# Kernel tuning notes

Hardware: AMD Instinct MI355X
Metric: run time of the kernel (lower is better)

The kernel has to match this reference:

```python
import jax, jax.numpy as jnp
import numpy as np

N = 4096      # sentences in document
K = 32        # clusters (args.k)
D = 256       # input_dim
H = 128       # hidden_dim
P_SAL = 0.5   # args.percent_sal


def setup_inputs() -> dict:
    key = jax.random.key(0)
    ks = jax.random.split(key, 12)
    s = 1.0 / np.sqrt(H)
    inp = {
        "sent_gae_embeds": jax.random.normal(ks[0], (N, D), jnp.float32),
        "labels": jax.random.randint(ks[1], (N,), 0, K),
        # GRU layer 0 (torch gate order r,z,n)
        "W_ih0": jax.random.uniform(ks[2], (3 * H, D), jnp.float32, -s, s),
        "W_hh0": jax.random.uniform(ks[3], (3 * H, H), jnp.float32, -s, s),
        "b_ih0": jax.random.uniform(ks[4], (3 * H,), jnp.float32, -s, s),
        "b_hh0": jax.random.uniform(ks[5], (3 * H,), jnp.float32, -s, s),
        # GRU layer 1
        "W_ih1": jax.random.uniform(ks[6], (3 * H, H), jnp.float32, -s, s),
        "W_hh1": jax.random.uniform(ks[7], (3 * H, H), jnp.float32, -s, s),
        "b_ih1": jax.random.uniform(ks[8], (3 * H,), jnp.float32, -s, s),
        "b_hh1": jax.random.uniform(ks[9], (3 * H,), jnp.float32, -s, s),
        # weight-normed linear: W = g * v / ||v|| (norm over input dim)
        "lin_v": jax.random.normal(ks[10], (1, D + H), jnp.float32) * 0.05,
        "lin_g": jnp.ones((1, 1), jnp.float32),
        "lin_b": jnp.zeros((1,), jnp.float32),
    }
    return inp


def _gru_layer(x, W_ih, W_hh, b_ih, b_hh):
    # x: [T, B, Din] -> outputs [T, B, H]
    xw = jnp.einsum("tbd,gd->tbg", x, W_ih) + b_ih  # precompute input gates

    def step(h, xw_t):
        hw = h @ W_hh.T + b_hh
        r = jax.nn.sigmoid(xw_t[:, :H] + hw[:, :H])
        z = jax.nn.sigmoid(xw_t[:, H:2 * H] + hw[:, H:2 * H])
        n = jnp.tanh(xw_t[:, 2 * H:] + r * hw[:, 2 * H:])
        h_new = (1.0 - z) * n + z * h
        return h_new, h_new

    h0 = jnp.zeros((x.shape[1], H), x.dtype)
    _, outs = jax.lax.scan(step, h0, xw)
    return outs


def reference(sent_gae_embeds, labels, W_ih0, W_hh0, b_ih0, b_hh0,
              W_ih1, W_hh1, b_ih1, b_hh1, lin_v, lin_g, lin_b):
    # --- cluster gather: position of each sentence within its cluster ---
    onehot = jax.nn.one_hot(labels, K, dtype=jnp.int32)          # [N, K]
    pos = jnp.cumsum(onehot, axis=0)[jnp.arange(N), labels] - 1  # [N]
    lengths = onehot.sum(axis=0)                                 # [K]

    # padded per-cluster sequences: [T=N, B=K, D]
    padded = jnp.zeros((N, K, D), sent_gae_embeds.dtype).at[pos, labels].set(sent_gae_embeds)

    # --- 2-layer GRU over each cluster sequence ---
    h1 = _gru_layer(padded, W_ih0, W_hh0, b_ih0, b_hh0)
    h2 = _gru_layer(h1, W_ih1, W_hh1, b_ih1, b_hh1)
    len_c = jnp.maximum(lengths, 1)  # empty cluster -> length-1 zero sequence
    cluster_embeds = h2[len_c - 1, jnp.arange(K)]  # [K, H]

    # --- scatter cluster embeds back onto sentences (sent detached as in torch) ---
    sent_d = jax.lax.stop_gradient(sent_gae_embeds)
    final_embeds = jnp.concatenate([sent_d, cluster_embeds[labels]], axis=-1)  # [N, D+H]

    # weight-normed linear + tanh
    Wn = lin_g * lin_v / jnp.linalg.norm(lin_v, axis=1, keepdims=True)
    scores = jnp.tanh(final_embeds @ Wn.T + lin_b)[:, 0]  # [N]

    # salience: per-cluster segment-sum normalization
    clu_scores = jax.ops.segment_sum(scores, labels, num_segments=K)
    sal_scores = scores / clu_scores[labels]

    # position scores: max(0.5, exp(-(i+1)/n**(1/3)))
    inv = np.float32(1.0 / (N ** (1.0 / 3.0)))
    pos_scores = jnp.maximum(0.5, jnp.exp(-(jnp.arange(N, dtype=jnp.float32) + 1.0) * inv))

    return P_SAL * sal_scores + (1.0 - P_SAL) * pos_scores
```

## Files before the change

kernel.cpp:

```cpp
#include <hip/hip_runtime.h>
#include <cmath>

#define NN 4096
#define KK 32
#define DD 256
#define HH 128
#define G3 384
#define CH 16
#define RH 136

typedef __attribute__((ext_vector_type(8))) _Float16 h8;
typedef __attribute__((ext_vector_type(4))) float f32x4;

__device__ __forceinline__ void bar_lds() {
  asm volatile("s_waitcnt lgkmcnt(0)" ::: "memory");
  __builtin_amdgcn_s_barrier();
}

__global__ __launch_bounds__(256) void prep_k(
    const int* __restrict__ labels, const float* __restrict__ lin_v,
    const float* __restrict__ lin_g,
    const float* __restrict__ Whh0, const float* __restrict__ Wih1,
    const float* __restrict__ Whh1,
    const float* __restrict__ sent, const float* __restrict__ W_ih0,
    const float* __restrict__ b_ih0,
    int* __restrict__ order, int* __restrict__ len, float* __restrict__ scale,
    _Float16* __restrict__ P, float* __restrict__ xw,
    float* __restrict__ sdot) {
  const int blk = blockIdx.x;
  const int t = threadIdx.x;
  if (blk < 72) {
    const int gid = blk * 256 + t;
    const int lane = gid & 63;
    const int kt = (gid >> 6) & 3;
    const int nt = (gid >> 8) % 24;
    const int mat = (gid >> 8) / 24;
    const float* W = (mat == 0) ? Whh0 : (mat == 1 ? Wih1 : Whh1);
    const int n = nt * 16 + (lane & 15);
    const int kbase = kt * 32 + (lane >> 4) * 8;
    _Float16* dst = P + (size_t)gid * 8;
#pragma unroll
    for (int j = 0; j < 8; ++j) dst[j] = (_Float16)W[(size_t)n * HH + kbase + j];
    return;
  }
  if (blk < 80) {
    const int wv = t >> 6, lane = t & 63;
    const int c = (blk - 72) * 4 + wv;
    int count = 0;
    for (int base = 0; base < NN; base += 64) {
      const int i = base + lane;
      const bool f = (labels[i] == c);
      const unsigned long long m = __ballot(f);
      if (f) order[c * NN + count + __popcll(m & ((1ull << lane) - 1ull))] = i;
      count += __popcll(m);
    }
    if (lane == 0) len[c] = count;
    return;
  }
  if (blk == 80) {
    if (t < 64) {
      float s = 0.f;
      for (int j = t; j < G3; j += 64) { const float v = lin_v[j]; s += v * v; }
      for (int off = 32; off; off >>= 1) s += __shfl_down(s, off);
      if (t == 0) scale[0] = lin_g[0] / sqrtf(s);
    }
    return;
  }
  if (blk >= 273) {
    const int b = blk - 273;
    const int wv = t >> 6, lane = t & 63;
    const float4 vv = *(const float4*)(lin_v + lane * 4);
    const int r0 = b * 64 + wv * 16;
    for (int rr = 0; rr < 16; ++rr) {
      const int r = r0 + rr;
      const float4 a = *(const float4*)(sent + (size_t)r * DD + lane * 4);
      float d = a.x * vv.x + a.y * vv.y + a.z * vv.z + a.w * vv.w;
      for (int off = 32; off; off >>= 1) d += __shfl_down(d, off);
      if (lane == 0) sdot[r] = d;
    }
    return;
  }
  __shared__ float Xs[16][132];
  __shared__ float Ws[16][68];
  const int g = blk - 81;
  const int i0 = (g & 31) * 128;
  const int g0 = (g >> 5) * 64;
  const int it = t & 15;
  const int gt = t >> 4;
  const int u0 = t * 2, u1 = t * 2 + 1;
  const int ra0 = u0 >> 2, ca0 = u0 & 3;
  const int ra1 = u1 >> 2, ca1 = u1 & 3;
  const int rw_ = t >> 2, cw_ = t & 3;
  float acc[8][4] = {};
  float4 x0, x1, w0;
  x0 = *(const float4*)(sent + (size_t)(i0 + ra0) * DD + ca0 * 4);
  x1 = *(const float4*)(sent + (size_t)(i0 + ra1) * DD + ca1 * 4);
  w0 = *(const float4*)(W_ih0 + (size_t)(g0 + rw_) * DD + cw_ * 4);
  for (int k0 = 0; k0 < DD; k0 += 16) {
    Xs[ca0 * 4 + 0][ra0] = x0.x; Xs[ca0 * 4 + 1][ra0] = x0.y;
    Xs[ca0 * 4 + 2][ra0] = x0.z; Xs[ca0 * 4 + 3][ra0] = x0.w;
    Xs[ca1 * 4 + 0][ra1] = x1.x; Xs[ca1 * 4 + 1][ra1] = x1.y;
    Xs[ca1 * 4 + 2][ra1] = x1.z; Xs[ca1 * 4 + 3][ra1] = x1.w;
    Ws[cw_ * 4 + 0][rw_] = w0.x; Ws[cw_ * 4 + 1][rw_] = w0.y;
    Ws[cw_ * 4 + 2][rw_] = w0.z; Ws[cw_ * 4 + 3][rw_] = w0.w;
    bar_lds();
    if (k0 + 16 < DD) {
      const int kn = k0 + 16;
      x0 = *(const float4*)(sent + (size_t)(i0 + ra0) * DD + kn + ca0 * 4);
      x1 = *(const float4*)(sent + (size_t)(i0 + ra1) * DD + kn + ca1 * 4);
      w0 = *(const float4*)(W_ih0 + (size_t)(g0 + rw_) * DD + kn + cw_ * 4);
    }
#pragma unroll
    for (int k = 0; k < 16; ++k) {
      float a[8], b[4];
#pragma unroll
      for (int x = 0; x < 8; ++x) a[x] = Xs[k][it * 8 + x];
#pragma unroll
      for (int y = 0; y < 4; ++y) b[y] = Ws[k][gt * 4 + y];
#pragma unroll
      for (int x = 0; x < 8; ++x)
#pragma unroll
        for (int y = 0; y < 4; ++y)
          acc[x][y] += a[x] * b[y];
    }
    bar_lds();
  }
  const float4 bs = *(const float4*)(b_ih0 + g0 + gt * 4);
#pragma unroll
  for (int x = 0; x < 8; ++x) {
    const int gi = i0 + it * 8 + x;
    float4 o;
    o.x = acc[x][0] + bs.x; o.y = acc[x][1] + bs.y;
    o.z = acc[x][2] + bs.z; o.w = acc[x][3] + bs.w;
    *(float4*)(xw + (size_t)gi * G3 + g0 + gt * 4) = o;
  }
}

__global__ __launch_bounds__(768) void gru_fused_k(
    const float* __restrict__ xw0,
    const _Float16* __restrict__ pack,
    const float* __restrict__ b_hh0, const float* __restrict__ b_ih0,
    const float* __restrict__ b_ih1, const float* __restrict__ b_hh1,
    const int* __restrict__ len, const int* __restrict__ order,
    const float* __restrict__ sdot,
    const float* __restrict__ lin_v, const float* __restrict__ scale,
    const float* __restrict__ lin_b, float* __restrict__ out) {
  const int c = blockIdx.x;
  const int t = threadIdx.x;
  const int wv = t >> 6, lane = t & 63;
  const int group = wv >> 2;
  const int v = wv & 3;
  h8 B[6][4];
  {
    const _Float16* mp = pack + (size_t)group * (24 * 4 * 64 * 8);
#pragma unroll
    for (int i = 0; i < 6; ++i) {
      const int nt = (i >> 1) * 8 + 2 * v + (i & 1);
#pragma unroll
      for (int kt = 0; kt < 4; ++kt)
        B[i][kt] = *(const h8*)(mp + ((size_t)(nt * 4 + kt) * 64 + lane) * 8);
    }
  }
  const int L = len[c];
  const int Lr = (L > 0) ? L : 1;
  const bool use_bih0 = (L == 0);
  const float4* const xsrc = (const float4*)xw0;
  const int u0 = t / 96, f0 = t - u0 * 96;
  const int u1 = (t + 768) / 96, f1 = (t + 768) - u1 * 96;
  const int tid1 = (wv - 4) * 64 + lane;
  int su[6], sf[6];
#pragma unroll
  for (int j = 0; j < 6; ++j) {
    const int e = tid1 + j * 256;
    su[j] = e / 96; sf[j] = e - su[j] * 96;
  }
  __shared__ __align__(16) float xwbuf[2 * CH * G3];
  __shared__ __align__(16) _Float16 ring[16][2 * RH];
  __shared__ __align__(16) _Float16 hp2[2][2][HH];
  __shared__ float xw1buf[2][8][G3];
  __shared__ float ce_s[HH];
  __shared__ float vbuf[HH];
  __shared__ float sc_s[2048];
  __shared__ float sc_red;
  {
    _Float16* rp = &ring[0][0];
    for (int u = t; u < 16 * 2 * RH; u += 768) rp[u] = (_Float16)0.f;
  }
  if (t < HH) {
    hp2[0][0][t] = (_Float16)0.f; hp2[0][1][t] = (_Float16)0.f;
    hp2[1][0][t] = (_Float16)0.f; hp2[1][1][t] = (_Float16)0.f;
  }
  if (!use_bih0) {
    float4* dst = (float4*)xwbuf;
    const int r0 = (u0 < L) ? order[c * NN + u0] : 0;
    const int r1 = (u1 < L) ? order[c * NN + u1] : 0;
    dst[t] = xsrc[(size_t)r0 * 96 + f0];
    dst[t + 768] = xsrc[(size_t)r1 * 96 + f1];
  }
  const int tg = 32 * v + (lane & 31);
  float bhr = 0.f, bhz = 0.f, bhn = 0.f;
  float bir = 0.f, biz = 0.f, bin = 0.f;
  float h = 0.f;
  if (lane < 32) {
    if (group == 0) {
      bhr = b_hh0[tg]; bhz = b_hh0[HH + tg]; bhn = b_hh0[2 * HH + tg];
      if (use_bih0) {
        bir = b_ih0[tg]; biz = b_ih0[HH + tg]; bin = b_ih0[2 * HH + tg];
      }
    } else if (group == 2) {
      bhr = b_hh1[tg]; bhz = b_hh1[HH + tg]; bhn = b_hh1[2 * HH + tg];
      bir = b_ih1[tg]; biz = b_ih1[HH + tg]; bin = b_ih1[2 * HH + tg];
    }
  }
  __syncthreads();
  const int q = lane >> 4;
  const int row = lane & 15;
  const int hs = (row == 0 || row == 4) ? 0 : 1;
  const bool hiacc = ((lane >> 4) & 1) != 0;
  float4 pf[6];
#pragma unroll
  for (int j = 0; j < 6; ++j) pf[j] = {0.f, 0.f, 0.f, 0.f};
  for (int it2 = 0; it2 < Lr + 9; ++it2) {
    const int par = it2 & 1;
    const int ph = it2 & (CH - 1);
    if (group == 0) {
      if (it2 < Lr) {
        __builtin_amdgcn_s_setprio(1);
        const _Float16* abse = &ring[(it2 - 1) & 15][hs * RH];
        h8 A[4];
#pragma unroll
        for (int kt = 0; kt < 4; ++kt)
          A[kt] = *(const h8*)(abse + kt * 32 + q * 8);
        float xr = bir, xz = biz, xn = bin;
        if (!use_bih0 && lane < 32) {
          const float* xrow = xwbuf + ((it2 >> 4) & 1) * (CH * G3)
                                    + (it2 & (CH - 1)) * G3;
          xr = xrow[tg]; xz = xrow[HH + tg]; xn = xrow[2 * HH + tg];
        }
        f32x4 a0[6];
#pragma unroll
        for (int i = 0; i < 6; ++i) {
          f32x4 aE = {0.f, 0.f, 0.f, 0.f};
          f32x4 aO = {0.f, 0.f, 0.f, 0.f};
          aE = __builtin_amdgcn_mfma_f32_16x16x32_f16(A[0], B[i][0], aE, 0, 0, 0);
          aO = __builtin_amdgcn_mfma_f32_16x16x32_f16(A[1], B[i][1], aO, 0, 0, 0);
          aE = __builtin_amdgcn_mfma_f32_16x16x32_f16(A[2], B[i][2], aE, 0, 0, 0);
          aO = __builtin_amdgcn_mfma_f32_16x16x32_f16(A[3], B[i][3], aO, 0, 0, 0);
          a0[i] = aE + aO;
        }
        if (lane < 32) {
          const float hwrA = a0[0][0] + a0[0][1], hwrB = a0[1][0] + a0[1][1];
          const float hwzA = a0[2][0] + a0[2][1], hwzB = a0[3][0] + a0[3][1];
          const float hwnA = a0[4][0] + a0[4][1], hwnB = a0[5][0] + a0[5][1];
          const float hwr = hiacc ? hwrB : hwrA;
          const float hwz = hiacc ? hwzB : hwzA;
          const float hwn = hiacc ? hwnB : hwnA;
          const float r = 1.f / (1.f + __expf(-(xr + bhr + hwr)));
          const float z = 1.f / (1.f + __expf(-(xz + bhz + hwz)));
          float tgt = xn + r * (bhn + hwn);
          tgt = fminf(fmaxf(tgt, -15.f), 15.f);
          const float e = __expf(2.f * tgt);
          const float n = (e - 1.f) / (e + 1.f);
          h = (1.f - z) * n + z * h;
          const _Float16 hi = (_Float16)h;
          _Float16* rs = &ring[it2 & 15][0];
          rs[tg] = hi;  rs[RH + tg] = (_Float16)(h - (float)hi);
        }
        __builtin_amdgcn_s_setprio(0);
      }
    } else if (group == 1) {
      if (!use_bih0) {
        if (ph == 2) {
          const int s = (it2 & ~(CH - 1)) + CH;
          if (s < Lr) {
#pragma unroll
            for (int j = 0; j < 6; ++j) {
              const int p = s + su[j];
              const int r = (p < L) ? order[c * NN + p] : 0;
              pf[j] = xsrc[(size_t)r * 96 + sf[j]];
            }
          }
        } else if (ph == 10) {
          const int s = (it2 & ~(CH - 1)) + CH;
          if (s < Lr) {
            float4* dst = (float4*)(xwbuf + (((s >> 4) & 1) ? CH * G3 : 0));
#pragma unroll
            for (int j = 0; j < 6; ++j) dst[tid1 + j * 256] = pf[j];
          }
        }
      }
      if (it2 >= 8 && (it2 & 7) == 0 && it2 - 8 < Lr) {
        const int c8 = it2 - 8;
        const int m = lane & 15;
        const int s = m >> 1, half = m & 1;
        const _Float16* abse = &ring[(c8 + s) & 15][half * RH];
        h8 A[4];
#pragma unroll
        for (int kt = 0; kt < 4; ++kt)
          A[kt] = *(const h8*)(abse + kt * 32 + q * 8);
        const int cbuf = (c8 >> 3) & 1;
        float* xo0 = &xw1buf[cbuf][2 * q][0];
        float* xo1 = &xw1buf[cbuf][2 * q + 1][0];
#pragma unroll
        for (int i = 0; i < 6; ++i) {
          f32x4 aE = {0.f, 0.f, 0.f, 0.f};
          f32x4 aO = {0.f, 0.f, 0.f, 0.f};
          aE = __builtin_amdgcn_mfma_f32_16x16x32_f16(A[0], B[i][0], aE, 0, 0, 0);
          aO = __builtin_amdgcn_mfma_f32_16x16x32_f16(A[1], B[i][1], aO, 0, 0, 0);
          aE = __builtin_amdgcn_mfma_f32_16x16x32_f16(A[2], B[i][2], aE, 0, 0, 0);
          aO = __builtin_amdgcn_mfma_f32_16x16x32_f16(A[3], B[i][3], aO, 0, 0, 0);
          const f32x4 a = aE + aO;
          const int nt = (i >> 1) * 8 + 2 * v + (i & 1);
          const int col = nt * 16 + (lane & 15);
          xo0[col] = a[0] + a[1];
          xo1[col] = a[2] + a[3];
        }
      }
    } else {
      if (it2 >= 9) {
        __builtin_amdgcn_s_setprio(1);
        const int j = it2 - 9;
        const _Float16* hbase = hp2[par][hs];
        h8 A[4];
#pragma unroll
        for (int kt = 0; kt < 4; ++kt)
          A[kt] = *(const h8*)(hbase + kt * 32 + q * 8);
        float xr = 0.f, xz = 0.f, xn = 0.f;
        if (lane < 32) {
          const float* xi = xw1buf[(j >> 3) & 1][j & 7];
          xr = xi[tg] + bir; xz = xi[HH + tg] + biz; xn = xi[2 * HH + tg] + bin;
        }
        f32x4 a1[6];
#pragma unroll
        for (int i = 0; i < 6; ++i) {
          f32x4 aE = {0.f, 0.f, 0.f, 0.f};
          f32x4 aO = {0.f, 0.f, 0.f, 0.f};
          aE = __builtin_amdgcn_mfma_f32_16x16x32_f16(A[0], B[i][0], aE, 0, 0, 0);
          aO = __builtin_amdgcn_mfma_f32_16x16x32_f16(A[1], B[i][1], aO, 0, 0, 0);
          aE = __builtin_amdgcn_mfma_f32_16x16x32_f16(A[2], B[i][2], aE, 0, 0, 0);
          aO = __builtin_amdgcn_mfma_f32_16x16x32_f16(A[3], B[i][3], aO, 0, 0, 0);
          a1[i] = aE + aO;
        }
        if (lane < 32) {
          const float hwrA = a1[0][0] + a1[0][1], hwrB = a1[1][0] + a1[1][1];
          const float hwzA = a1[2][0] + a1[2][1], hwzB = a1[3][0] + a1[3][1];
          const float hwnA = a1[4][0] + a1[4][1], hwnB = a1[5][0] + a1[5][1];
          const float hwr = hiacc ? hwrB : hwrA;
          const float hwz = hiacc ? hwzB : hwzA;
          const float hwn = hiacc ? hwnB : hwnA;
          const float r = 1.f / (1.f + __expf(-(xr + bhr + hwr)));
          const float z = 1.f / (1.f + __expf(-(xz + bhz + hwz)));
          float tgt = xn + r * (bhn + hwn);
          tgt = fminf(fmaxf(tgt, -15.f), 15.f);
          const float e = __expf(2.f * tgt);
          const float n = (e - 1.f) / (e + 1.f);
          h = (1.f - z) * n + z * h;
          const _Float16 hi = (_Float16)h;
          hp2[par ^ 1][0][tg] = hi;
          hp2[par ^ 1][1][tg] = (_Float16)(h - (float)hi);
        }
        __builtin_amdgcn_s_setprio(0);
      }
    }
    bar_lds();
  }
  if (L == 0) return;
  if (group == 2 && lane < 32) ce_s[tg] = h;
  if (t < HH) vbuf[t] = lin_v[DD + t];
  __syncthreads();
  if (wv == 0) {
    float cd = ce_s[lane] * vbuf[lane] + ce_s[64 + lane] * vbuf[64 + lane];
    for (int off = 32; off; off >>= 1) cd += __shfl_down(cd, off);
    if (lane == 0) sc_red = cd;
  }
  __syncthreads();
  const float cedot = sc_red;
  const float sc = scale[0], lb = lin_b[0];
  const int Lc = (L < 2048) ? L : 2048;
  for (int p = t; p < Lc; p += 768) {
    const int i = order[c * NN + p];
    sc_s[p] = tanhf(sc * (sdot[i] + cedot) + lb);
  }
  __syncthreads();
  if (wv == 0) {
    float s = 0.f;
    for (int p = lane; p < Lc; p += 64) s += sc_s[p];
    for (int off = 32; off; off >>= 1) s += __shfl_down(s, off);
    if (lane == 0) sc_red = 1.f / s;
  }
  __syncthreads();
  const float inv = sc_red;
  for (int p = t; p < Lc; p += 768) {
    const int i = order[c * NN + p];
    float ps = __expf(-(float)(i + 1) * 0.0625f);
    ps = fmaxf(0.5f, ps);
    out[i] = 0.5f * (sc_s[p] * inv) + 0.5f * ps;
  }
}

extern "C" void kernel_launch(void* const* d_in, const int* in_sizes, int n_in,
                              void* d_out, int out_size, void* d_ws, size_t ws_size,
                              hipStream_t stream) {
  const float* sent   = (const float*)d_in[0];
  const int*   labels = (const int*)d_in[1];
  const float* W_ih0  = (const float*)d_in[2];
  const float* W_hh0  = (const float*)d_in[3];
  const float* b_ih0  = (const float*)d_in[4];
  const float* b_hh0  = (const float*)d_in[5];
  const float* W_ih1  = (const float*)d_in[6];
  const float* W_hh1  = (const float*)d_in[7];
  const float* b_ih1  = (const float*)d_in[8];
  const float* b_hh1  = (const float*)d_in[9];
  const float* lin_v  = (const float*)d_in[10];
  const float* lin_g  = (const float*)d_in[11];
  const float* lin_b  = (const float*)d_in[12];
  float* out = (float*)d_out;

  char* ws = (char*)d_ws;
  size_t off = 0;
  auto alloc = [&](size_t bytes) -> void* {
    void* p = ws + off;
    off = (off + bytes + 255) & ~(size_t)255;
    return p;
  };
  int*   order  = (int*)  alloc((size_t)KK * NN * sizeof(int));
  int*   len    = (int*)  alloc(KK * sizeof(int));
  float* scale  = (float*)alloc(sizeof(float));
  _Float16* pack = (_Float16*)alloc((size_t)18432 * 8 * sizeof(_Float16));
  float* xw     = (float*)alloc((size_t)NN * G3 * sizeof(float));
  float* sdot   = (float*)alloc((size_t)NN * sizeof(float));
  (void)ws_size; (void)in_sizes; (void)n_in; (void)out_size;

  prep_k<<<dim3(337), dim3(256), 0, stream>>>(
      labels, lin_v, lin_g, W_hh0, W_ih1, W_hh1,
      sent, W_ih0, b_ih0, order, len, scale, pack, xw, sdot);
  gru_fused_k<<<dim3(KK), dim3(768), 0, stream>>>(
      xw, pack, b_hh0, b_ih0, b_ih1, b_hh1, len, order,
      sdot, lin_v, scale, lin_b, out);
}
```

Before: 276.7 us.

## Prefetch layer-0 input gates via direct global-to-LDS loads and cache cluster order in LDS

The prefetch warps now issue global_load_lds DMA loads for the next chunk of precomputed layer-0 input gates straight into the LDS double buffer, instead of staging them in registers and writing them out later. A vmcnt wait at the end of each chunk phase guards completion. The cluster's order index list is copied into shared memory once at the start, so the gather and the epilogue no longer read it from global memory. This frees registers in the prefetch group and shortens the address-dependency chain, but adds 16KB of LDS, which could reduce occupancy. It also depends on the wait and barrier ordering being correct for the DMA writes.

New measurement: 250.8 us. 9.4% less time.

```diff
diff --git a/kernel.cpp b/kernel.cpp
--- a/kernel.cpp
+++ b/kernel.cpp
@@ -15,6 +15,13 @@
 __device__ __forceinline__ void bar_lds() {
   asm volatile("s_waitcnt lgkmcnt(0)" ::: "memory");
   __builtin_amdgcn_s_barrier();
+}
+
+__device__ __forceinline__ void gload_lds16(const float4* g, float4* l) {
+  __builtin_amdgcn_global_load_lds(
+      (const __attribute__((address_space(1))) void*)g,
+      (__attribute__((address_space(3))) void*)l,
+      16, 0, 0);
 }
 
 __global__ __launch_bounds__(256) void prep_k(
@@ -168,16 +175,11 @@
   const int u0 = t / 96, f0 = t - u0 * 96;
   const int u1 = (t + 768) / 96, f1 = (t + 768) - u1 * 96;
   const int tid1 = (wv - 4) * 64 + lane;
-  int su[6], sf[6];
-#pragma unroll
-  for (int j = 0; j < 6; ++j) {
-    const int e = tid1 + j * 256;
-    su[j] = e / 96; sf[j] = e - su[j] * 96;
-  }
   __shared__ __align__(16) float xwbuf[2 * CH * G3];
   __shared__ __align__(16) _Float16 ring[16][2 * RH];
   __shared__ __align__(16) _Float16 hp2[2][2][HH];
   __shared__ float xw1buf[2][8][G3];
+  __shared__ int order_s[NN];
   __shared__ float ce_s[HH];
   __shared__ float vbuf[HH];
   __shared__ float sc_s[2048];
@@ -190,6 +192,7 @@
     hp2[0][0][t] = (_Float16)0.f; hp2[0][1][t] = (_Float16)0.f;
     hp2[1][0][t] = (_Float16)0.f; hp2[1][1][t] = (_Float16)0.f;
   }
+  for (int i = t; i < L; i += 768) order_s[i] = order[c * NN + i];
   if (!use_bih0) {
     float4* dst = (float4*)xwbuf;
     const int r0 = (u0 < L) ? order[c * NN + u0] : 0;
@@ -217,9 +220,6 @@
   const int row = lane & 15;
   const int hs = (row == 0 || row == 4) ? 0 : 1;
   const bool hiacc = ((lane >> 4) & 1) != 0;
-  float4 pf[6];
-#pragma unroll
-  for (int j = 0; j < 6; ++j) pf[j] = {0.f, 0.f, 0.f, 0.f};
   for (int it2 = 0; it2 < Lr + 9; ++it2) {
     const int par = it2 & 1;
     const int ph = it2 & (CH - 1);
@@ -269,23 +269,18 @@
         __builtin_amdgcn_s_setprio(0);
       }
     } else if (group == 1) {
-      if (!use_bih0) {
-        if (ph == 2) {
-          const int s = (it2 & ~(CH - 1)) + CH;
-          if (s < Lr) {
-#pragma unroll
-            for (int j = 0; j < 6; ++j) {
-              const int p = s + su[j];
-              const int r = (p < L) ? order[c * NN + p] : 0;
-              pf[j] = xsrc[(size_t)r * 96 + sf[j]];
-            }
-          }
-        } else if (ph == 10) {
-          const int s = (it2 & ~(CH - 1)) + CH;
-          if (s < Lr) {
-            float4* dst = (float4*)(xwbuf + (((s >> 4) & 1) ? CH * G3 : 0));
-#pragma unroll
-            for (int j = 0; j < 6; ++j) dst[tid1 + j * 256] = pf[j];
+      if (!use_bih0 && ph == 2) {
+        const int s = (it2 & ~(CH - 1)) + CH;
+        if (s < Lr) {
+          float4* dst = (float4*)(xwbuf + (((s >> 4) & 1) ? CH * G3 : 0));
+          const int w1 = wv - 4;
+#pragma unroll
+          for (int j = 0; j < 6; ++j) {
+            const int e = tid1 + j * 256;
+            const int u = e / 96, f = e - u * 96;
+            const int p = s + u;
+            const int r = (p < L) ? order_s[p] : 0;
+            gload_lds16(xsrc + (size_t)r * 96 + f, dst + j * 256 + w1 * 64);
           }
         }
       }
@@ -316,6 +311,8 @@
           xo1[col] = a[2] + a[3];
         }
       }
+      if (!use_bih0 && ph == 15)
+        asm volatile("s_waitcnt vmcnt(0)" ::: "memory");
     } else {
       if (it2 >= 9) {
         __builtin_amdgcn_s_setprio(1);
@@ -378,7 +375,7 @@
   const float sc = scale[0], lb = lin_b[0];
   const int Lc = (L < 2048) ? L : 2048;
   for (int p = t; p < Lc; p += 768) {
-    const int i = order[c * NN + p];
+    const int i = order_s[p];
     sc_s[p] = tanhf(sc * (sdot[i] + cedot) + lb);
   }
   __syncthreads();
@@ -391,7 +388,7 @@
   __syncthreads();
   const float inv = sc_red;
   for (int p = t; p < Lc; p += 768) {
-    const int i = order[c * NN + p];
+    const int i = order_s[p];
     float ps = __expf(-(float)(i + 1) * 0.0625f);
     ps = fmaxf(0.5f, ps);
     out[i] = 0.5f * (sc_s[p] * inv) + 0.5f * ps;
```
